# Optimization experiments

Hardware: AMD Instinct MI355X
Metric: run time of the kernel (lower is better)

The kernel has to match this reference:

```python
import jax, jax.numpy as jnp
import numpy as np

B, C, L = 8, 512, 2048


def setup_inputs() -> dict:
    key = jax.random.key(0)
    ks = jax.random.split(key, 7)
    s = 1.0 / np.sqrt(C)
    return {
        "x": jax.random.normal(ks[0], (B, C, L), dtype=jnp.float32),
        "Wq": jax.random.normal(ks[1], (C, C), dtype=jnp.float32) * s,
        "bq": jax.random.normal(ks[2], (C,), dtype=jnp.float32) * s,
        "Wk": jax.random.normal(ks[3], (C, C), dtype=jnp.float32) * s,
        "bk": jax.random.normal(ks[4], (C,), dtype=jnp.float32) * s,
        "Wv": jax.random.normal(ks[5], (C, C), dtype=jnp.float32) * s,
        "bv": jax.random.normal(ks[6], (C,), dtype=jnp.float32) * s,
    }


def reference(x, Wq, bq, Wk, bk, Wv, bv):
    # Conv1d(kernel_size=1) == per-position linear: [C_out, C_in] @ x[b,:,l]
    q = jnp.einsum('oi,bil->bol', Wq, x) + bq[None, :, None]  # [B, C, L]
    k = jnp.einsum('oi,bil->bol', Wk, x) + bk[None, :, None]
    v = jnp.einsum('oi,bil->bol', Wv, x) + bv[None, :, None]
    scale = 1.0 / jnp.sqrt(jnp.asarray(x.shape[1], dtype=x.dtype))
    # scores[b, l, m] = sum_c q[b,c,l] * k[b,c,m] / sqrt(C)
    scores = jnp.einsum('bcl,bcm->blm', q, k) * scale  # [B, L, L]
    attn = jax.nn.softmax(scores, axis=-1)
    # out[b, c, l] = sum_m v[b,c,m] * attn[b,l,m]   (== bmm(V, attn^T))
    return jnp.einsum('bcm,blm->bcl', v, attn)  # [B, C, L]
```

## Files before the change

kernel.cpp:

```cpp
#include <hip/hip_runtime.h>
#include <hip/hip_bf16.h>
#include <math.h>

#define B 8
#define C 512
#define L 2048

using bf16x8 = __bf16 __attribute__((ext_vector_type(8)));
using f32x4  = float __attribute__((ext_vector_type(4)));

#define MFMA(a, b, c) __builtin_amdgcn_mfma_f32_16x16x32_bf16((a), (b), (c), 0, 0, 0)
#define SC2 0.06375872f
#define SH2 -17.312340f

__device__ __forceinline__ unsigned short f2bf(float f) {
    unsigned int u; __builtin_memcpy(&u, &f, 4);
    u += 0x7FFF + ((u >> 16) & 1);
    return (unsigned short)(u >> 16);
}
__device__ __forceinline__ void load_lds16(const unsigned short* g, unsigned short* l) {
    __builtin_amdgcn_global_load_lds(
        (const __attribute__((address_space(1))) unsigned int*)g,
        (__attribute__((address_space(3))) unsigned int*)l, 16, 0, 0);
}

template<int MODE, int KDIM>
__device__ __forceinline__ void gemm_core(
    const unsigned short* __restrict__ A,
    const unsigned short* __restrict__ Bm,
    unsigned short* As, unsigned short* Bs,
    void* __restrict__ OutV, int ldo,
    float* __restrict__ ep)
{
    const int t = threadIdx.x;
    const int wave = t >> 6, lane = t & 63;
    const int ll = t & 15, quad = (t >> 4) & 3;
    const int lr = lane >> 2, chunk = lane & 3;
    const int wm = (wave & 1) * 64, wn = (wave >> 1) * 64;

    const unsigned short* gA0 = A  + (size_t)(wave * 32 + lr) * KDIM + chunk * 8;
    const unsigned short* gB0 = Bm + (size_t)(wave * 32 + lr) * KDIM + chunk * 8;
    unsigned short* lA0 = As + (wave * 32) * 32;
    unsigned short* lB0 = Bs + (wave * 32) * 32;
    const int P1 = 128 * 32;

    f32x4 acc[4][4];
#pragma unroll
    for (int i = 0; i < 4; ++i)
#pragma unroll
        for (int j = 0; j < 4; ++j) acc[i][j] = (f32x4){0.f, 0.f, 0.f, 0.f};

#pragma unroll 1
    for (int k0 = 0; k0 < KDIM; k0 += 64) {
        __syncthreads();
        load_lds16(gA0 + k0, lA0);
        load_lds16(gA0 + (size_t)16 * KDIM + k0, lA0 + 16 * 32);
        load_lds16(gA0 + k0 + 32, lA0 + P1);
        load_lds16(gA0 + (size_t)16 * KDIM + k0 + 32, lA0 + P1 + 16 * 32);
        load_lds16(gB0 + k0, lB0);
        load_lds16(gB0 + (size_t)16 * KDIM + k0, lB0 + 16 * 32);
        load_lds16(gB0 + k0 + 32, lB0 + P1);
        load_lds16(gB0 + (size_t)16 * KDIM + k0 + 32, lB0 + P1 + 16 * 32);
        __syncthreads();

#pragma unroll
        for (int p = 0; p < 2; ++p) {
            bf16x8 af[4], bf[4];
#pragma unroll
            for (int mi = 0; mi < 4; ++mi)
                af[mi] = *(const bf16x8*)&As[p * P1 + (wm + mi * 16 + ll) * 32 + quad * 8];
#pragma unroll
            for (int ni = 0; ni < 4; ++ni)
                bf[ni] = *(const bf16x8*)&Bs[p * P1 + (wn + ni * 16 + ll) * 32 + quad * 8];
#pragma unroll
            for (int mi = 0; mi < 4; ++mi)
#pragma unroll
                for (int ni = 0; ni < 4; ++ni)
                    acc[mi][ni] = MFMA(af[mi], bf[ni], acc[mi][ni]);
        }
    }

#pragma unroll
    for (int mi = 0; mi < 4; ++mi)
#pragma unroll
        for (int ni = 0; ni < 4; ++ni) {
            const int col = wn + ni * 16 + ll;
            float epc = 0.f;
            if (MODE == 0) epc = ep[col];
            if (MODE == 3) epc = 1.0f / ep[col];
#pragma unroll
            for (int r = 0; r < 4; ++r) {
                const int row = wm + mi * 16 + quad * 4 + r;
                float v = acc[mi][ni][r];
                if (MODE == 0)      v += epc;
                else if (MODE == 1) v += ep[row];
                else                v *= epc;
                if (MODE == 3)
                    ((float*)OutV)[(size_t)row * ldo + col] = v;
                else
                    ((unsigned short*)OutV)[(size_t)row * ldo + col] = f2bf(v);
            }
        }
}

__global__ __launch_bounds__(256) void xpose_cvt(
    const float* __restrict__ x, unsigned short* __restrict__ xt)
{
    __shared__ float tile[64][69];
    const int b = blockIdx.z, l0 = blockIdx.x * 64, c0 = blockIdx.y * 64;
    const int t = threadIdx.x;
    const int lx = t & 15, cy = t >> 4;
    const float* xb = x + (size_t)b * C * L;
#pragma unroll
    for (int p = 0; p < 4; ++p) {
        float4 v = *(const float4*)(xb + (size_t)(c0 + p * 16 + cy) * L + l0 + lx * 4);
        tile[p * 16 + cy][lx * 4 + 0] = v.x;
        tile[p * 16 + cy][lx * 4 + 1] = v.y;
        tile[p * 16 + cy][lx * 4 + 2] = v.z;
        tile[p * 16 + cy][lx * 4 + 3] = v.w;
    }
    __syncthreads();
    const int ocl = t & 15, ot = t >> 4;
    unsigned short* xtb = xt + (size_t)b * L * C;
#pragma unroll
    for (int p = 0; p < 4; ++p) {
        int ol = p * 16 + ot;
        union { unsigned short h[4]; uint2 u; } pk;
#pragma unroll
        for (int i = 0; i < 4; ++i) pk.h[i] = f2bf(tile[ocl * 4 + i][ol]);
        *(uint2*)(xtb + (size_t)(l0 + ol) * C + c0 + ocl * 4) = pk.u;
    }
}

__global__ __launch_bounds__(256) void wcvt(
    const float* __restrict__ Wq, const float* __restrict__ Wk,
    const float* __restrict__ Wv, unsigned short* __restrict__ o,
    float* __restrict__ rsum)
{
    if (blockIdx.x < 16) {
        float4 z = make_float4(0.f, 0.f, 0.f, 0.f);
        *(float4*)(rsum + (blockIdx.x * 256 + threadIdx.x) * 4) = z;
    }
    const int i = (blockIdx.x * 256 + threadIdx.x) * 4;
    const int which = i >> 18;
    const int off = i & 0x3FFFF;
    const float* src = (which == 0) ? Wq : (which == 1) ? Wk : Wv;
    float4 v = *(const float4*)(src + off);
    union { unsigned short h[4]; uint2 u; } pk;
    pk.h[0] = f2bf(v.x); pk.h[1] = f2bf(v.y); pk.h[2] = f2bf(v.z); pk.h[3] = f2bf(v.w);
    *(uint2*)(o + i) = pk.u;
}

__global__ __launch_bounds__(256) void qkv_gemm(
    const unsigned short* __restrict__ xt, const unsigned short* __restrict__ Wb,
    const float* __restrict__ bq, const float* __restrict__ bk,
    const float* __restrict__ bv,
    unsigned short* __restrict__ Qt, unsigned short* __restrict__ Kt,
    unsigned short* __restrict__ Vv)
{
    __shared__ unsigned short As[2 * 128 * 32], Bs[2 * 128 * 32];
    const int id = blockIdx.x;
    const int b = id & 7, r = id >> 3;
    const int which = r >> 6, tt = r & 63;
    const unsigned short* xtb = xt + (size_t)b * L * C;
    if (which < 2) {
        const int m0 = (tt & 15) * 128, n0 = (tt >> 4) * 128;
        const unsigned short* A  = xtb + (size_t)m0 * C;
        const unsigned short* Bm = Wb + (size_t)which * C * C + (size_t)n0 * C;
        unsigned short* Out = (which ? Kt : Qt) + (size_t)b * L * C
                              + (size_t)m0 * C + n0;
        gemm_core<0, C>(A, Bm, As, Bs, Out, C,
                        const_cast<float*>((which ? bk : bq) + n0));
    } else {
        const int m0 = (tt & 3) * 128, n0 = (tt >> 2) * 128;
        const unsigned short* A  = Wb + (size_t)2 * C * C + (size_t)m0 * C;
        const unsigned short* Bm = xtb + (size_t)n0 * C;
        unsigned short* Out = Vv + (size_t)b * C * L + (size_t)m0 * L + n0;
        gemm_core<1, C>(A, Bm, As, Bs, Out, L, const_cast<float*>(bv + m0));
    }
}

__global__ __launch_bounds__(512, 4) void sc_exp3(
    const unsigned short* __restrict__ Qt, const unsigned short* __restrict__ Kt,
    unsigned short* __restrict__ P, float* __restrict__ rsum,
    int hoff, int qrows, int mshift)
{
    __shared__ unsigned short As[256 * 64];
    __shared__ unsigned short Bs[128 * 64];
    constexpr int KD = C;

    const int id = blockIdx.x;
    const int b = id & 7, rr = id >> 3;
    const int m0 = (rr & ((1 << mshift) - 1)) * 256, n0 = (rr >> mshift) * 128;
    const unsigned short* A  = Qt + (size_t)b * L * C + (size_t)(hoff + m0) * C;
    const unsigned short* Bm = Kt + (size_t)b * L * C + (size_t)n0 * C;
    unsigned short* Out = P + (size_t)b * qrows * L + (size_t)m0 * L + n0;
    float* ep = rsum + (size_t)b * L + hoff + m0;

    const int t = threadIdx.x;
    const int wave = t >> 6;
    const int ll = t & 15, quad = (t >> 4) & 3;
    const int wm = (wave & 3) * 64, wn = (wave >> 2) * 64;

    const int r0 = t >> 3;
    const int swz = ((t & 7) ^ (r0 & 7)) * 8;
    const unsigned short* gA = A  + (size_t)r0 * KD + swz;
    const unsigned short* gB = Bm + (size_t)r0 * KD + swz;
    unsigned short* lA = As + wave * 512;
    unsigned short* lB = Bs + wave * 512;

    const int sw8 = ll & 7;

    f32x4 acc[4][4];
#pragma unroll
    for (int i = 0; i < 4; ++i)
#pragma unroll
        for (int j = 0; j < 4; ++j) acc[i][j] = (f32x4){0.f, 0.f, 0.f, 0.f};

#pragma unroll 1
    for (int k0 = 0; k0 < KD; k0 += 64) {
        __syncthreads();
        load_lds16(gA + k0,                     lA);
        load_lds16(gA + (size_t)64  * KD + k0,  lA + 64 * 64);
        load_lds16(gA + (size_t)128 * KD + k0,  lA + 128 * 64);
        load_lds16(gA + (size_t)192 * KD + k0,  lA + 192 * 64);
        load_lds16(gB + k0,                     lB);
        load_lds16(gB + (size_t)64  * KD + k0,  lB + 64 * 64);
        __syncthreads();

#pragma unroll
        for (int p = 0; p < 2; ++p) {
            bf16x8 af[4], bf[4];
#pragma unroll
            for (int mi = 0; mi < 4; ++mi)
                af[mi] = *(const bf16x8*)&As[(wm + mi * 16 + ll) * 64
                                             + ((p * 4 + quad) ^ sw8) * 8];
#pragma unroll
            for (int ni = 0; ni < 4; ++ni)
                bf[ni] = *(const bf16x8*)&Bs[(wn + ni * 16 + ll) * 64
                                             + ((p * 4 + quad) ^ sw8) * 8];
#pragma unroll
            for (int mi = 0; mi < 4; ++mi)
#pragma unroll
                for (int ni = 0; ni < 4; ++ni)
                    acc[mi][ni] = MFMA(af[mi], bf[ni], acc[mi][ni]);
        }
    }

    float rpart[4][4];
#pragma unroll
    for (int mi = 0; mi < 4; ++mi)
#pragma unroll
        for (int r = 0; r < 4; ++r) rpart[mi][r] = 0.f;

#pragma unroll
    for (int mi = 0; mi < 4; ++mi)
#pragma unroll
        for (int ni = 0; ni < 4; ++ni) {
            const int col = wn + ni * 16 + ll;
#pragma unroll
            for (int r = 0; r < 4; ++r) {
                const int row = wm + mi * 16 + quad * 4 + r;
                float v = exp2f(fmaf(acc[mi][ni][r], SC2, SH2));
                rpart[mi][r] += v;
                Out[(size_t)row * L + col] = f2bf(v);
            }
        }
#pragma unroll
    for (int mi = 0; mi < 4; ++mi)
#pragma unroll
        for (int r = 0; r < 4; ++r) {
            float s = rpart[mi][r];
            s += __shfl_xor(s, 1, 64);
            s += __shfl_xor(s, 2, 64);
            s += __shfl_xor(s, 4, 64);
            s += __shfl_xor(s, 8, 64);
            if (ll == 0) atomicAdd(ep + wm + mi * 16 + quad * 4 + r, s);
        }
}

__global__ __launch_bounds__(256) void pv_gemm(
    const unsigned short* __restrict__ Vv, const unsigned short* __restrict__ P,
    const float* __restrict__ rsum, float* __restrict__ out,
    int hoff, int qrows)
{
    __shared__ unsigned short As[2 * 128 * 32], Bs[2 * 128 * 32];
    const int id = blockIdx.x;
    const int b = id & 7, r = id >> 3;
    const int m0 = (r & 3) * 128, n0 = (r >> 2) * 128;
    const unsigned short* A  = Vv + (size_t)b * C * L + (size_t)m0 * L;
    const unsigned short* Bm = P + (size_t)b * qrows * L + (size_t)n0 * L;
    float* Out = out + (size_t)b * C * L + (size_t)m0 * L + hoff + n0;
    float* ep = const_cast<float*>(rsum) + (size_t)b * L + hoff + n0;
    gemm_core<3, L>(A, Bm, As, Bs, Out, L, ep);
}

extern "C" void kernel_launch(void* const* d_in, const int* in_sizes, int n_in,
                              void* d_out, int out_size, void* d_ws, size_t ws_size,
                              hipStream_t stream) {
    const float* x  = (const float*)d_in[0];
    const float* Wq = (const float*)d_in[1];
    const float* bq = (const float*)d_in[2];
    const float* Wk = (const float*)d_in[3];
    const float* bk = (const float*)d_in[4];
    const float* Wv = (const float*)d_in[5];
    const float* bv = (const float*)d_in[6];
    float* out = (float*)d_out;

    const size_t BCL = (size_t)B * C * L;
    const bool fullP = ws_size >= 119078912ull;

    unsigned short* Qt = (unsigned short*)d_ws;
    unsigned short* Kt = Qt + BCL;
    unsigned short* Vv = Kt + BCL;
    unsigned short *Wb, *xt, *P;
    float* rsum;
    if (fullP) {
        Wb   = Vv + BCL;
        rsum = (float*)(Wb + (size_t)3 * C * C);
        xt   = (unsigned short*)(rsum + (size_t)B * L);
        P    = xt;
    } else {
        xt   = Vv + BCL;
        P    = xt;
        Wb   = P + (size_t)B * 1024 * L;
        rsum = (float*)(Wb + (size_t)3 * C * C);
    }

    xpose_cvt<<<dim3(L / 64, C / 64, B), 256, 0, stream>>>(x, xt);
    wcvt<<<dim3(3 * C * C / 1024), 256, 0, stream>>>(Wq, Wk, Wv, Wb, rsum);
    qkv_gemm<<<dim3(1536), 256, 0, stream>>>(xt, Wb, bq, bk, bv, Qt, Kt, Vv);

    if (fullP) {
        sc_exp3<<<dim3(1024), 512, 0, stream>>>(Qt, Kt, P, rsum, 0, L, 3);
        pv_gemm<<<dim3(512), 256, 0, stream>>>(Vv, P, rsum, out, 0, L);
    } else {
        for (int h = 0; h < 2; ++h) {
            sc_exp3<<<dim3(512), 512, 0, stream>>>(Qt, Kt, P, rsum, h * 1024, 1024, 2);
            pv_gemm<<<dim3(256), 256, 0, stream>>>(Vv, P, rsum, out, h * 1024, 1024);
        }
    }
}
```

Baseline: 220.2 us.

## Fuse score-exp and PV GEMM into one persistent kernel with grid barrier

Merges the weight conversion and x transpose into a single prep kernel, and replaces the separate sc_exp3 and pv_gemm launches with one sc_pv kernel of 512 blocks. Each block computes two score tiles, then waits on a global atomic-counter barrier before running the PV GEMM. The counter is reset inside qkv_gemm. This removes launch overhead and inter-kernel gaps, but it relies on all 512 blocks being co-resident, or the barrier deadlocks. It also changes the PV tiling to 512-thread blocks with a 128x128 output tile.

```diff
diff --git a/kernel.cpp b/kernel.cpp
--- a/kernel.cpp
+++ b/kernel.cpp
@@ -12,6 +12,8 @@
 #define MFMA(a, b, c) __builtin_amdgcn_mfma_f32_16x16x32_bf16((a), (b), (c), 0, 0, 0)
 #define SC2 0.06375872f
 #define SH2 -17.312340f
+
+__device__ unsigned g_ctr;
 
 __device__ __forceinline__ unsigned short f2bf(float f) {
     unsigned int u; __builtin_memcpy(&u, &f, 4);
@@ -103,12 +105,32 @@
         }
 }
 
-__global__ __launch_bounds__(256) void xpose_cvt(
-    const float* __restrict__ x, unsigned short* __restrict__ xt)
+__global__ __launch_bounds__(256) void prep(
+    const float* __restrict__ x, const float* __restrict__ Wq,
+    const float* __restrict__ Wk, const float* __restrict__ Wv,
+    unsigned short* __restrict__ xt, unsigned short* __restrict__ o,
+    float* __restrict__ rsum)
 {
     __shared__ float tile[64][69];
+    const int t = threadIdx.x;
+    const int flat = blockIdx.x + 32 * (blockIdx.y + 8 * blockIdx.z);
+
+    if (flat < 768) {
+        if (flat < 16) {
+            float4 z = make_float4(0.f, 0.f, 0.f, 0.f);
+            *(float4*)(rsum + (flat * 256 + t) * 4) = z;
+        }
+        const int i = (flat * 256 + t) * 4;
+        const int which = i >> 18;
+        const int off = i & 0x3FFFF;
+        const float* src = (which == 0) ? Wq : (which == 1) ? Wk : Wv;
+        float4 v = *(const float4*)(src + off);
+        union { unsigned short h[4]; uint2 u; } pk;
+        pk.h[0] = f2bf(v.x); pk.h[1] = f2bf(v.y); pk.h[2] = f2bf(v.z); pk.h[3] = f2bf(v.w);
+        *(uint2*)(o + i) = pk.u;
+    }
+
     const int b = blockIdx.z, l0 = blockIdx.x * 64, c0 = blockIdx.y * 64;
-    const int t = threadIdx.x;
     const int lx = t & 15, cy = t >> 4;
     const float* xb = x + (size_t)b * C * L;
 #pragma unroll
@@ -130,25 +152,6 @@
         for (int i = 0; i < 4; ++i) pk.h[i] = f2bf(tile[ocl * 4 + i][ol]);
         *(uint2*)(xtb + (size_t)(l0 + ol) * C + c0 + ocl * 4) = pk.u;
     }
-}
-
-__global__ __launch_bounds__(256) void wcvt(
-    const float* __restrict__ Wq, const float* __restrict__ Wk,
-    const float* __restrict__ Wv, unsigned short* __restrict__ o,
-    float* __restrict__ rsum)
-{
-    if (blockIdx.x < 16) {
-        float4 z = make_float4(0.f, 0.f, 0.f, 0.f);
-        *(float4*)(rsum + (blockIdx.x * 256 + threadIdx.x) * 4) = z;
-    }
-    const int i = (blockIdx.x * 256 + threadIdx.x) * 4;
-    const int which = i >> 18;
-    const int off = i & 0x3FFFF;
-    const float* src = (which == 0) ? Wq : (which == 1) ? Wk : Wv;
-    float4 v = *(const float4*)(src + off);
-    union { unsigned short h[4]; uint2 u; } pk;
-    pk.h[0] = f2bf(v.x); pk.h[1] = f2bf(v.y); pk.h[2] = f2bf(v.z); pk.h[3] = f2bf(v.w);
-    *(uint2*)(o + i) = pk.u;
 }
 
 __global__ __launch_bounds__(256) void qkv_gemm(
@@ -159,6 +162,8 @@
     unsigned short* __restrict__ Vv)
 {
     __shared__ unsigned short As[2 * 128 * 32], Bs[2 * 128 * 32];
+    if (blockIdx.x == 0 && threadIdx.x == 0)
+        __hip_atomic_store(&g_ctr, 0u, __ATOMIC_RELAXED, __HIP_MEMORY_SCOPE_AGENT);
     const int id = blockIdx.x;
     const int b = id & 7, r = id >> 3;
     const int which = r >> 6, tt = r & 63;
@@ -180,6 +185,179 @@
     }
 }
 
+__global__ __launch_bounds__(512, 4) void sc_pv(
+    const unsigned short* __restrict__ Qt, const unsigned short* __restrict__ Kt,
+    const unsigned short* __restrict__ Vv, unsigned short* __restrict__ P,
+    float* __restrict__ rsum, float* __restrict__ out)
+{
+    __shared__ unsigned short As[256 * 64];
+    __shared__ unsigned short Bs[128 * 64];
+
+    const int id = blockIdx.x;
+    const int b = id & 7, rr = id >> 3;
+    const int t = threadIdx.x;
+    const int wave = t >> 6;
+    const int ll = t & 15, quad = (t >> 4) & 3;
+    const int r0 = t >> 3;
+    const int swz = ((t & 7) ^ (r0 & 7)) * 8;
+    const int sw8 = ll & 7;
+
+    {
+        const int n0 = (rr & 15) * 128, mp = rr >> 4;
+        const unsigned short* gB = Kt + (size_t)b * L * C
+                                   + (size_t)(n0 + r0) * C + swz;
+        const int wm = (wave & 3) * 64, wn = (wave >> 2) * 64;
+        unsigned short* lA = As + wave * 512;
+        unsigned short* lB = Bs + wave * 512;
+
+#pragma unroll 1
+        for (int s = 0; s < 2; ++s) {
+            const int m0 = (mp * 2 + s) * 256;
+            const unsigned short* gA = Qt + (size_t)b * L * C
+                                       + (size_t)(m0 + r0) * C + swz;
+            unsigned short* Out = P + (size_t)b * L * L + (size_t)m0 * L + n0;
+            float* ep = rsum + (size_t)b * L + m0;
+
+            f32x4 acc[4][4];
+#pragma unroll
+            for (int i = 0; i < 4; ++i)
+#pragma unroll
+                for (int j = 0; j < 4; ++j) acc[i][j] = (f32x4){0.f, 0.f, 0.f, 0.f};
+
+#pragma unroll 1
+            for (int k0 = 0; k0 < C; k0 += 64) {
+                __syncthreads();
+                load_lds16(gA + k0,                    lA);
+                load_lds16(gA + (size_t)64  * C + k0,  lA + 64 * 64);
+                load_lds16(gA + (size_t)128 * C + k0,  lA + 128 * 64);
+                load_lds16(gA + (size_t)192 * C + k0,  lA + 192 * 64);
+                load_lds16(gB + k0,                    lB);
+                load_lds16(gB + (size_t)64  * C + k0,  lB + 64 * 64);
+                __syncthreads();
+#pragma unroll
+                for (int p = 0; p < 2; ++p) {
+                    bf16x8 af[4], bf[4];
+#pragma unroll
+                    for (int mi = 0; mi < 4; ++mi)
+                        af[mi] = *(const bf16x8*)&As[(wm + mi * 16 + ll) * 64
+                                                     + ((p * 4 + quad) ^ sw8) * 8];
+#pragma unroll
+                    for (int ni = 0; ni < 4; ++ni)
+                        bf[ni] = *(const bf16x8*)&Bs[(wn + ni * 16 + ll) * 64
+                                                     + ((p * 4 + quad) ^ sw8) * 8];
+#pragma unroll
+                    for (int mi = 0; mi < 4; ++mi)
+#pragma unroll
+                        for (int ni = 0; ni < 4; ++ni)
+                            acc[mi][ni] = MFMA(af[mi], bf[ni], acc[mi][ni]);
+                }
+            }
+
+            float rpart[4][4];
+#pragma unroll
+            for (int mi = 0; mi < 4; ++mi)
+#pragma unroll
+                for (int r = 0; r < 4; ++r) rpart[mi][r] = 0.f;
+#pragma unroll
+            for (int mi = 0; mi < 4; ++mi)
+#pragma unroll
+                for (int ni = 0; ni < 4; ++ni) {
+                    const int col = wn + ni * 16 + ll;
+#pragma unroll
+                    for (int r = 0; r < 4; ++r) {
+                        const int row = wm + mi * 16 + quad * 4 + r;
+                        float v = exp2f(fmaf(acc[mi][ni][r], SC2, SH2));
+                        rpart[mi][r] += v;
+                        Out[(size_t)row * L + col] = f2bf(v);
+                    }
+                }
+#pragma unroll
+            for (int mi = 0; mi < 4; ++mi)
+#pragma unroll
+                for (int r = 0; r < 4; ++r) {
+                    float s2 = rpart[mi][r];
+                    s2 += __shfl_xor(s2, 1, 64);
+                    s2 += __shfl_xor(s2, 2, 64);
+                    s2 += __shfl_xor(s2, 4, 64);
+                    s2 += __shfl_xor(s2, 8, 64);
+                    if (ll == 0) atomicAdd(ep + wm + mi * 16 + quad * 4 + r, s2);
+                }
+        }
+    }
+
+    __syncthreads();
+    __threadfence();
+    if (t == 0) {
+        atomicAdd(&g_ctr, 1u);
+        while (__hip_atomic_load(&g_ctr, __ATOMIC_RELAXED,
+                                 __HIP_MEMORY_SCOPE_AGENT) < 512u)
+            __builtin_amdgcn_s_sleep(2);
+    }
+    __syncthreads();
+    __threadfence();
+
+    {
+        const int m0 = (rr & 3) * 128, n0 = (rr >> 2) * 128;
+        const unsigned short* gA = Vv + (size_t)b * C * L
+                                   + (size_t)(m0 + r0) * L + swz;
+        const unsigned short* gB = P + (size_t)b * L * L
+                                   + (size_t)(n0 + r0) * L + swz;
+        float* Out = out + (size_t)b * C * L + (size_t)m0 * L + n0;
+        const float* ep = rsum + (size_t)b * L + n0;
+        const int wm = (wave & 1) * 64, wn = (wave >> 1) * 32;
+        unsigned short* lAa = As + wave * 512;
+        unsigned short* lAb = As + 4096 + wave * 512;
+        unsigned short* lBa = Bs + wave * 512;
+        unsigned short* lBb = Bs + 4096 + wave * 512;
+
+        f32x4 acc[4][2];
+#pragma unroll
+        for (int i = 0; i < 4; ++i)
+#pragma unroll
+            for (int j = 0; j < 2; ++j) acc[i][j] = (f32x4){0.f, 0.f, 0.f, 0.f};
+
+#pragma unroll 1
+        for (int k0 = 0; k0 < L; k0 += 64) {
+            __syncthreads();
+            load_lds16(gA + k0,                   lAa);
+            load_lds16(gA + (size_t)64 * L + k0,  lAb);
+            load_lds16(gB + k0,                   lBa);
+            load_lds16(gB + (size_t)64 * L + k0,  lBb);
+            __syncthreads();
+#pragma unroll
+            for (int p = 0; p < 2; ++p) {
+                bf16x8 af[4], bf[2];
+#pragma unroll
+                for (int mi = 0; mi < 4; ++mi)
+                    af[mi] = *(const bf16x8*)&As[(wm + mi * 16 + ll) * 64
+                                                 + ((p * 4 + quad) ^ sw8) * 8];
+#pragma unroll
+                for (int ni = 0; ni < 2; ++ni)
+                    bf[ni] = *(const bf16x8*)&Bs[(wn + ni * 16 + ll) * 64
+                                                 + ((p * 4 + quad) ^ sw8) * 8];
+#pragma unroll
+                for (int mi = 0; mi < 4; ++mi)
+#pragma unroll
+                    for (int ni = 0; ni < 2; ++ni)
+                        acc[mi][ni] = MFMA(af[mi], bf[ni], acc[mi][ni]);
+            }
+        }
+
+#pragma unroll
+        for (int mi = 0; mi < 4; ++mi)
+#pragma unroll
+            for (int ni = 0; ni < 2; ++ni) {
+                const int col = wn + ni * 16 + ll;
+                const float inv = 1.0f / ep[col];
+#pragma unroll
+                for (int r = 0; r < 4; ++r) {
+                    const int row = wm + mi * 16 + quad * 4 + r;
+                    Out[(size_t)row * L + col] = acc[mi][ni][r] * inv;
+                }
+            }
+    }
+}
+
 __global__ __launch_bounds__(512, 4) void sc_exp3(
     const unsigned short* __restrict__ Qt, const unsigned short* __restrict__ Kt,
     unsigned short* __restrict__ P, float* __restrict__ rsum,
@@ -201,14 +379,12 @@
     const int wave = t >> 6;
     const int ll = t & 15, quad = (t >> 4) & 3;
     const int wm = (wave & 3) * 64, wn = (wave >> 2) * 64;
-
     const int r0 = t >> 3;
     const int swz = ((t & 7) ^ (r0 & 7)) * 8;
     const unsigned short* gA = A  + (size_t)r0 * KD + swz;
     const unsigned short* gB = Bm + (size_t)r0 * KD + swz;
     unsigned short* lA = As + wave * 512;
     unsigned short* lB = Bs + wave * 512;
-
     const int sw8 = ll & 7;
 
     f32x4 acc[4][4];
@@ -227,7 +403,6 @@
         load_lds16(gB + k0,                     lB);
         load_lds16(gB + (size_t)64  * KD + k0,  lB + 64 * 64);
         __syncthreads();
-
 #pragma unroll
         for (int p = 0; p < 2; ++p) {
             bf16x8 af[4], bf[4];
@@ -252,7 +427,6 @@
     for (int mi = 0; mi < 4; ++mi)
 #pragma unroll
         for (int r = 0; r < 4; ++r) rpart[mi][r] = 0.f;
-
 #pragma unroll
     for (int mi = 0; mi < 4; ++mi)
 #pragma unroll
@@ -327,13 +501,11 @@
         rsum = (float*)(Wb + (size_t)3 * C * C);
     }
 
-    xpose_cvt<<<dim3(L / 64, C / 64, B), 256, 0, stream>>>(x, xt);
-    wcvt<<<dim3(3 * C * C / 1024), 256, 0, stream>>>(Wq, Wk, Wv, Wb, rsum);
+    prep<<<dim3(L / 64, C / 64, B), 256, 0, stream>>>(x, Wq, Wk, Wv, xt, Wb, rsum);
     qkv_gemm<<<dim3(1536), 256, 0, stream>>>(xt, Wb, bq, bk, bv, Qt, Kt, Vv);
 
     if (fullP) {
-        sc_exp3<<<dim3(1024), 512, 0, stream>>>(Qt, Kt, P, rsum, 0, L, 3);
-        pv_gemm<<<dim3(512), 256, 0, stream>>>(Vv, P, rsum, out, 0, L);
+        sc_pv<<<dim3(512), 512, 0, stream>>>(Qt, Kt, Vv, P, rsum, out);
     } else {
         for (int h = 0; h < 2; ++h) {
             sc_exp3<<<dim3(512), 512, 0, stream>>>(Qt, Kt, P, rsum, h * 1024, 1024, 2);
```

Result: slower. 451.9 us (+105.2%).

## Merge prep kernels and stage exp scores through LDS for wide stores

Applied to the files above, without the earlier changes.

Combines the x transpose/convert and the weight convert plus rsum zeroing into one prep kernel, removing a launch. In sc_exp3, the bf16 exp values are paired via lane shuffles, written to per-wave LDS scratch, then read back as rows and stored to global P with 16-byte coalesced writes instead of scattered 2-byte stores. This adds an extra barrier, LDS traffic and shuffles in the epilogue.

```diff
diff --git a/kernel.cpp b/kernel.cpp
--- a/kernel.cpp
+++ b/kernel.cpp
@@ -103,12 +103,32 @@
         }
 }
 
-__global__ __launch_bounds__(256) void xpose_cvt(
-    const float* __restrict__ x, unsigned short* __restrict__ xt)
+__global__ __launch_bounds__(256) void prep(
+    const float* __restrict__ x, const float* __restrict__ Wq,
+    const float* __restrict__ Wk, const float* __restrict__ Wv,
+    unsigned short* __restrict__ xt, unsigned short* __restrict__ o,
+    float* __restrict__ rsum)
 {
     __shared__ float tile[64][69];
+    const int t = threadIdx.x;
+    const int flat = blockIdx.x + 32 * (blockIdx.y + 8 * blockIdx.z);
+
+    if (flat < 768) {
+        if (flat < 16) {
+            float4 z = make_float4(0.f, 0.f, 0.f, 0.f);
+            *(float4*)(rsum + (flat * 256 + t) * 4) = z;
+        }
+        const int i = (flat * 256 + t) * 4;
+        const int which = i >> 18;
+        const int off = i & 0x3FFFF;
+        const float* src = (which == 0) ? Wq : (which == 1) ? Wk : Wv;
+        float4 v = *(const float4*)(src + off);
+        union { unsigned short h[4]; uint2 u; } pk;
+        pk.h[0] = f2bf(v.x); pk.h[1] = f2bf(v.y); pk.h[2] = f2bf(v.z); pk.h[3] = f2bf(v.w);
+        *(uint2*)(o + i) = pk.u;
+    }
+
     const int b = blockIdx.z, l0 = blockIdx.x * 64, c0 = blockIdx.y * 64;
-    const int t = threadIdx.x;
     const int lx = t & 15, cy = t >> 4;
     const float* xb = x + (size_t)b * C * L;
 #pragma unroll
@@ -130,25 +150,6 @@
         for (int i = 0; i < 4; ++i) pk.h[i] = f2bf(tile[ocl * 4 + i][ol]);
         *(uint2*)(xtb + (size_t)(l0 + ol) * C + c0 + ocl * 4) = pk.u;
     }
-}
-
-__global__ __launch_bounds__(256) void wcvt(
-    const float* __restrict__ Wq, const float* __restrict__ Wk,
-    const float* __restrict__ Wv, unsigned short* __restrict__ o,
-    float* __restrict__ rsum)
-{
-    if (blockIdx.x < 16) {
-        float4 z = make_float4(0.f, 0.f, 0.f, 0.f);
-        *(float4*)(rsum + (blockIdx.x * 256 + threadIdx.x) * 4) = z;
-    }
-    const int i = (blockIdx.x * 256 + threadIdx.x) * 4;
-    const int which = i >> 18;
-    const int off = i & 0x3FFFF;
-    const float* src = (which == 0) ? Wq : (which == 1) ? Wk : Wv;
-    float4 v = *(const float4*)(src + off);
-    union { unsigned short h[4]; uint2 u; } pk;
-    pk.h[0] = f2bf(v.x); pk.h[1] = f2bf(v.y); pk.h[2] = f2bf(v.z); pk.h[3] = f2bf(v.w);
-    *(uint2*)(o + i) = pk.u;
 }
 
 __global__ __launch_bounds__(256) void qkv_gemm(
@@ -198,7 +199,7 @@
     float* ep = rsum + (size_t)b * L + hoff + m0;
 
     const int t = threadIdx.x;
-    const int wave = t >> 6;
+    const int wave = t >> 6, lane = t & 63;
     const int ll = t & 15, quad = (t >> 4) & 3;
     const int wm = (wave & 3) * 64, wn = (wave >> 2) * 64;
 
@@ -208,7 +209,6 @@
     const unsigned short* gB = Bm + (size_t)r0 * KD + swz;
     unsigned short* lA = As + wave * 512;
     unsigned short* lB = Bs + wave * 512;
-
     const int sw8 = ll & 7;
 
     f32x4 acc[4][4];
@@ -247,6 +247,9 @@
         }
     }
 
+    __syncthreads();
+    unsigned* scratch = (unsigned*)As + wave * 1024;
+
     float rpart[4][4];
 #pragma unroll
     for (int mi = 0; mi < 4; ++mi)
@@ -254,18 +257,35 @@
         for (int r = 0; r < 4; ++r) rpart[mi][r] = 0.f;
 
 #pragma unroll
-    for (int mi = 0; mi < 4; ++mi)
-#pragma unroll
-        for (int ni = 0; ni < 4; ++ni) {
-            const int col = wn + ni * 16 + ll;
-#pragma unroll
-            for (int r = 0; r < 4; ++r) {
-                const int row = wm + mi * 16 + quad * 4 + r;
-                float v = exp2f(fmaf(acc[mi][ni][r], SC2, SH2));
-                rpart[mi][r] += v;
-                Out[(size_t)row * L + col] = f2bf(v);
-            }
-        }
+    for (int h = 0; h < 2; ++h) {
+#pragma unroll
+        for (int mi2 = 0; mi2 < 2; ++mi2) {
+            const int mi = h * 2 + mi2;
+#pragma unroll
+            for (int ni = 0; ni < 4; ++ni)
+#pragma unroll
+                for (int r = 0; r < 4; ++r) {
+                    float v = exp2f(fmaf(acc[mi][ni][r], SC2, SH2));
+                    rpart[mi][r] += v;
+                    unsigned bfv = f2bf(v);
+                    unsigned pvv = (unsigned)__shfl_xor((int)bfv, 1, 64);
+                    unsigned packed = (ll & 1) ? ((pvv & 0xFFFFu) | (bfv << 16))
+                                               : ((bfv & 0xFFFFu) | (pvv << 16));
+                    if (!(ll & 1))
+                        scratch[(mi2 * 16 + quad * 4 + r) * 32 + ni * 8 + (ll >> 1)]
+                            = packed;
+                }
+        }
+#pragma unroll
+        for (int i = 0; i < 4; ++i) {
+            const int rl = i * 8 + (lane >> 3);
+            uint4 d = *(const uint4*)(scratch + rl * 32 + (lane & 7) * 4);
+            const int row = wm + h * 32 + rl;
+            const int col = wn + (lane & 7) * 8;
+            *(uint4*)&Out[(size_t)row * L + col] = d;
+        }
+    }
+
 #pragma unroll
     for (int mi = 0; mi < 4; ++mi)
 #pragma unroll
@@ -327,8 +347,7 @@
         rsum = (float*)(Wb + (size_t)3 * C * C);
     }
 
-    xpose_cvt<<<dim3(L / 64, C / 64, B), 256, 0, stream>>>(x, xt);
-    wcvt<<<dim3(3 * C * C / 1024), 256, 0, stream>>>(Wq, Wk, Wv, Wb, rsum);
+    prep<<<dim3(L / 64, C / 64, B), 256, 0, stream>>>(x, Wq, Wk, Wv, xt, Wb, rsum);
     qkv_gemm<<<dim3(1536), 256, 0, stream>>>(xt, Wb, bq, bk, bv, Qt, Kt, Vv);
 
     if (fullP) {
```

New measurement: 233.0 us. 5.8% more time.
